# Kernel optimization log

Measured on AMD Instinct MI355X. Metric: run time of the kernel, lower is better.

Reference implementation:

```python
import jax, jax.numpy as jnp
import numpy as np

B, I, H, S = 16384, 256, 256, 32
EVENT_THRESH = 0.85


def setup_inputs() -> dict:
    key = jax.random.key(0)
    ks = jax.random.split(key, 20)
    r = lambda k, shp: jax.random.normal(k, shp, dtype=jnp.float32)
    w = lambda k, shp: jax.random.normal(k, shp, dtype=jnp.float32) * 0.02
    return {
        # forward args / state
        "x_t": r(ks[0], (B, I)),
        "h_lstm": r(ks[1], (B, H)),
        "c_lstm": r(ks[2], (B, H)),
        "h_mem_prev": jnp.zeros((B, H), jnp.float32),
        "slots": r(ks[3], (B, S, I)),
        "ptr": jax.random.randint(ks[4], (B,), 0, S, dtype=jnp.int64),
        # SequenceMemoryCell params (weights stored as (in, out))
        "W_val": w(ks[5], (I, I)),
        "b_val": jnp.zeros((I,), jnp.float32),
        "W_ev": w(ks[6], (I, 1)),
        "b_ev": jnp.zeros((1,), jnp.float32),
        "pos_emb": r(ks[7], (S, I)),
        "slot_weights": jnp.ones((S,), jnp.float32),
        "W_sp": w(ks[8], (I, H)),
        "b_sp": jnp.zeros((H,), jnp.float32),
        # LSTM params
        "W_ih": w(ks[9], (I + H, 4 * H)),
        "b_ih": jnp.zeros((4 * H,), jnp.float32),
        "W_hh": w(ks[10], (H, 4 * H)),
    }


def reference(x_t, h_lstm, c_lstm, h_mem_prev, slots, ptr,
              W_val, b_val, W_ev, b_ev, pos_emb, slot_weights, W_sp, b_sp,
              W_ih, b_ih, W_hh):
    n_slots = slot_weights.shape[0]
    # --- SequenceMemoryCell ---
    e_t = jax.nn.sigmoid(x_t @ W_ev + b_ev)            # (B, 1)
    v = x_t @ W_val + b_val                            # (B, I)
    event_mask = e_t[:, 0] > EVENT_THRESH              # (B,)
    # circular-buffer scatter write at ptr, gated by event_mask
    onehot = jnp.arange(n_slots)[None, :] == ptr[:, None]          # (B, S)
    write = event_mask[:, None] & onehot                           # (B, S)
    new_slots = jnp.where(write[:, :, None], v[:, None, :], slots) # (B, S, I)
    new_ptr = (ptr + event_mask.astype(ptr.dtype)) % n_slots
    # weighted pool over slots with positional embeddings
    w = jax.nn.softmax(slot_weights)                               # (S,)
    pooled = jnp.einsum('bsi,s->bi', new_slots + pos_emb[None], w) # (B, I)
    h_mem = pooled @ W_sp + b_sp                                   # (B, H)
    # --- LSTM on [x_t; h_mem] ---
    gates = jnp.concatenate([x_t, h_mem], axis=1) @ W_ih + b_ih + h_lstm @ W_hh
    i_g, f_g, g_t, o_g = jnp.split(gates, 4, axis=1)
    c_new = jax.nn.sigmoid(f_g) * c_lstm + jax.nn.sigmoid(i_g) * jnp.tanh(g_t)
    h_new = jax.nn.sigmoid(o_g) * jnp.tanh(c_new)
    return (h_new, c_new, h_mem, new_slots, new_ptr)
```

## Files before the change

kernel.cpp:

```cpp
#include <hip/hip_runtime.h>
#include <hip/hip_bf16.h>

#define B_SZ 16384
#define I_SZ 256
#define H_SZ 256
#define S_SZ 32

typedef __attribute__((ext_vector_type(8))) short short8;
typedef __attribute__((ext_vector_type(4))) float f32x4;

__device__ __forceinline__ ushort f2b(float f) {
  __hip_bfloat16 h = __float2bfloat16(f);
  return *reinterpret_cast<ushort*>(&h);
}
__device__ __forceinline__ float sgm(float x) { return 1.0f / (1.0f + expf(-x)); }

__device__ __forceinline__ void gll16(const void* g, void* l) {
  __builtin_amdgcn_global_load_lds(
      (const __attribute__((address_space(1))) unsigned*)g,
      (__attribute__((address_space(3))) unsigned*)l, 16, 0, 0);
}

__global__ __launch_bounds__(256) void prep_pe(
    const float* __restrict__ slot_w, const float* __restrict__ pos_emb,
    float* __restrict__ wsm_g, float* __restrict__ pe_g) {
  int t = threadIdx.x;
  __shared__ float w_sh[32];
  if (t < 32) {
    float v = slot_w[t];
    float m = v;
#pragma unroll
    for (int off = 16; off; off >>= 1) m = fmaxf(m, __shfl_xor(m, off));
    float e = expf(v - m);
    float s2 = e;
#pragma unroll
    for (int off = 16; off; off >>= 1) s2 += __shfl_xor(s2, off);
    float wv = e / s2;
    w_sh[t] = wv;
    wsm_g[t] = wv;
  }
  __syncthreads();
  float accp = 0.f;
#pragma unroll 8
  for (int s = 0; s < 32; s++) accp += w_sh[s] * pos_emb[s * 256 + t];
  pe_g[t] = accp;
}

__global__ __launch_bounds__(256, 6) void front(
    const float* __restrict__ x_t, const float* __restrict__ h_lstm,
    const float* __restrict__ slots, const int* __restrict__ ptr,
    const float* __restrict__ W_val, const float* __restrict__ b_val,
    const float* __restrict__ W_ev, const float* __restrict__ b_ev,
    const float* __restrict__ slot_w,
    const float* __restrict__ W_sp, const float* __restrict__ W_ih,
    const float* __restrict__ W_hh, const float* __restrict__ b_ih,
    const float* __restrict__ b_sp, const float* __restrict__ wsm_g,
    const float* __restrict__ pe_g,
    float* __restrict__ out_slots, float* __restrict__ out_ptr,
    ushort* __restrict__ x_b, ushort* __restrict__ hl_b,
    ushort* __restrict__ pooled_b, ushort* __restrict__ WspT,
    ushort* __restrict__ WcatT, float* __restrict__ biasp) {
  __shared__ float x_sh[4][256];
  __shared__ float w_sh[32];
  const int bid = blockIdx.x;
  const int t = threadIdx.x;

  if (bid < 4096) {
    int l = t & 63;
    int w = t >> 6;
    int b = bid * 4 + w;

    if (t < 32) w_sh[t] = wsm_g[t];
    f32x4 pev = *(const f32x4*)(pe_g + l * 4);

    float4 x4 = *(const float4*)(x_t + (size_t)b * 256 + l * 4);
    *(float4*)&x_sh[w][l * 4] = x4;
    ushort4 xb = make_ushort4(f2b(x4.x), f2b(x4.y), f2b(x4.z), f2b(x4.w));
    *(ushort4*)&x_b[(size_t)b * 256 + l * 4] = xb;
    float4 hl4 = *(const float4*)(h_lstm + (size_t)b * 256 + l * 4);
    ushort4 hb = make_ushort4(f2b(hl4.x), f2b(hl4.y), f2b(hl4.z), f2b(hl4.w));
    *(ushort4*)&hl_b[(size_t)b * 256 + l * 4] = hb;

    float4 we4 = *(const float4*)(W_ev + l * 4);
    float p = x4.x * we4.x + x4.y * we4.y + x4.z * we4.z + x4.w * we4.w;
    for (int off = 32; off; off >>= 1) p += __shfl_xor(p, off, 64);
    float z = p + b_ev[0];
    bool ev = sgm(z) > 0.85f;
    int pb = ptr[b];
    if (l == 0) out_ptr[b] = (float)(ev ? ((pb + 1) & 31) : pb);

    __syncthreads();

    f32x4 v4 = {0.f, 0.f, 0.f, 0.f};
    if (ev) {
      v4 = *(const f32x4*)(b_val + l * 4);
      for (int k = 0; k < 256; k++) {
        float xv = x_sh[w][k];
        f32x4 wv = *(const f32x4*)(W_val + (size_t)k * 256 + l * 4);
        v4 += xv * wv;
      }
    }

    const f32x4* sl4 = (const f32x4*)slots + (size_t)b * 2048;
    f32x4* os4 = (f32x4*)out_slots + (size_t)b * 2048;
    f32x4 pool = {0.f, 0.f, 0.f, 0.f};
#pragma unroll 8
    for (int s = 0; s < 32; s++) {
      f32x4 tv = __builtin_nontemporal_load(sl4 + s * 64 + l);
      if (ev && s == pb) tv = v4;
      __builtin_nontemporal_store(tv, os4 + s * 64 + l);
      pool += w_sh[s] * tv;
    }
    pool += pev;
    ushort4 pb4 = make_ushort4(f2b(pool[0]), f2b(pool[1]), f2b(pool[2]), f2b(pool[3]));
    *(ushort4*)&pooled_b[(size_t)b * 256 + l * 4] = pb4;

  } else if (bid < 4104) {
    for (int e = (bid - 4096) * 256 + t; e < 65536; e += 8 * 256) {
      int n = e >> 8, k = e & 255;
      WspT[e] = f2b(W_sp[k * 256 + n]);
    }
  } else if (bid < 4168) {
    for (int e = (bid - 4104) * 256 + t; e < 1024 * 512; e += 64 * 256) {
      int r = e >> 9, kk = e & 511;
      int k = (kk < 256) ? kk : kk + 256;
      int hb = r >> 6, g = (r >> 4) & 3, hl = r & 15;
      int n = g * 256 + hb * 16 + hl;
      float v = (k < 512) ? W_ih[(size_t)k * 1024 + n]
                          : W_hh[(size_t)(k - 512) * 1024 + n];
      WcatT[(size_t)r * 768 + k] = f2b(v);
    }
  } else if (bid < 4424) {
    int i = bid - 4168;
    x_sh[0][t] = W_sp[(size_t)i * 256 + t];
    __syncthreads();
    int n0 = t * 4;
    f32x4 acc = {0.f, 0.f, 0.f, 0.f};
    for (int m = 0; m < 256; m++) {
      float s = x_sh[0][m];
      f32x4 w2 = *(const f32x4*)(W_ih + (size_t)(256 + m) * 1024 + n0);
      acc += s * w2;
    }
#pragma unroll
    for (int d = 0; d < 4; d++) {
      int n = n0 + d;
      int g = n >> 8, rem = n & 255, hb = rem >> 4, hl = rem & 15;
      int r = hb * 64 + g * 16 + hl;
      WcatT[(size_t)r * 768 + 256 + i] = f2b(acc[d]);
    }
  } else {
    int n0 = t * 4;
    f32x4 acc = *(const f32x4*)(b_ih + n0);
    for (int m = 0; m < 256; m++) {
      float s = b_sp[m];
      f32x4 w2 = *(const f32x4*)(W_ih + (size_t)(256 + m) * 1024 + n0);
      acc += s * w2;
    }
    *(f32x4*)(biasp + n0) = acc;
  }
}

__global__ __launch_bounds__(256) void gemm_hmem(
    const ushort* __restrict__ A0, const ushort* __restrict__ WT,
    const float* __restrict__ bias, float* __restrict__ out_f32) {
  int l = threadIdx.x & 63;
  int wid = threadIdx.x >> 6;
  int wm = wid >> 1, wn = wid & 1;
  int m0 = blockIdx.x * 128;
  int n0 = blockIdx.y * 128;
  __shared__ ushort Ash[128 * 32];
  __shared__ ushort Bsh[128 * 32];

  f32x4 acc[4][4] = {};

  for (int k0 = 0; k0 < 256; k0 += 32) {
#pragma unroll
    for (int i = 0; i < 2; i++) {
      int seg = i * 256 + threadIdx.x;
      int row = seg >> 2, cb = (seg & 3) * 8;
      gll16(A0 + (size_t)(m0 + row) * 256 + k0 + cb, Ash + seg * 8);
    }
#pragma unroll
    for (int i = 0; i < 2; i++) {
      int seg = i * 256 + threadIdx.x;
      int row = seg >> 2, cb = (seg & 3) * 8;
      gll16(WT + (size_t)(n0 + row) * 256 + k0 + cb, Bsh + seg * 8);
    }
    __syncthreads();

    short8 af[4], bfr[4];
#pragma unroll
    for (int m = 0; m < 4; m++)
      af[m] = *(const short8*)&Ash[(wm * 64 + m * 16 + (l & 15)) * 32 + (l >> 4) * 8];
#pragma unroll
    for (int n = 0; n < 4; n++)
      bfr[n] = *(const short8*)&Bsh[(wn * 64 + n * 16 + (l & 15)) * 32 + (l >> 4) * 8];
#pragma unroll
    for (int m = 0; m < 4; m++)
#pragma unroll
      for (int n = 0; n < 4; n++)
        acc[m][n] = __builtin_amdgcn_mfma_f32_16x16x32_bf16(af[m], bfr[n], acc[m][n], 0, 0, 0);
    __syncthreads();
  }

#pragma unroll
  for (int m = 0; m < 4; m++)
#pragma unroll
    for (int n = 0; n < 4; n++)
#pragma unroll
      for (int r = 0; r < 4; r++) {
        int row = m0 + wm * 64 + m * 16 + (l >> 4) * 4 + r;
        int col = n0 + wn * 64 + n * 16 + (l & 15);
        out_f32[(size_t)row * 256 + col] = acc[m][n][r] + bias[col];
      }
}

template <int KTOT>
__global__ __launch_bounds__(512) void gemm256_lstm(
    const ushort* __restrict__ A0s, const ushort* __restrict__ A1s,
    const ushort* __restrict__ A2s, const ushort* __restrict__ WT,
    const float* __restrict__ bias, const float* __restrict__ c_lstm,
    float* __restrict__ h_out, float* __restrict__ c_out) {
  constexpr int NT = KTOT / 64;
  __shared__ ushort Ash[2][2][128][64];
  __shared__ ushort Bsh[2][2][128][64];
  const int tid = threadIdx.x;
  const int l = tid & 63;
  const int wid = tid >> 6;
  const int wm = wid >> 2, wn = wid & 3;
  const int id = blockIdx.x;
  const int xcd = id & 7, jj = id >> 3;
  const int mb = xcd * 8 + (jj >> 2), nb = jj & 3;
  const int m0 = mb * 256, n0 = nb * 256;

  auto asel = [&](int kt) { return kt < 4 ? A0s : (kt < 8 ? A1s : A2s); };

  auto stageA = [&](int bu, int h, int kt) {
    const ushort* s = asel(kt);
    int cb = (kt & 3) * 64;
#pragma unroll
    for (int ld = 0; ld < 2; ld++) {
      int seg = ld * 512 + tid;
      int row = seg >> 3, C = seg & 7;
      int Cs = C ^ (row & 7);
      gll16(s + (size_t)(m0 + h * 128 + row) * 256 + cb + Cs * 8,
            &Ash[bu][h][0][0] + seg * 8);
    }
  };
  auto stageB = [&](int bu, int h, int kt) {
    int cb = kt * 64;
#pragma unroll
    for (int ld = 0; ld < 2; ld++) {
      int seg = ld * 512 + tid;
      int row = seg >> 3, C = seg & 7;
      int Cs = C ^ (row & 7);
      gll16(WT + (size_t)(n0 + h * 128 + row) * KTOT + cb + Cs * 8,
            &Bsh[bu][h][0][0] + seg * 8);
    }
  };

  f32x4 acc[8][4] = {};

  stageB(0, 0, 0); stageB(0, 1, 0);
  stageA(0, 0, 0); stageA(0, 1, 0);
  stageB(1, 0, 1); stageB(1, 1, 1);

  for (int t = 0; t < NT; t++) {
    const int c = t & 1;
    const ushort* Abase = &Ash[c][wm][0][0];
    const ushort* Bbase = &Bsh[c][wn >> 1][0][0];

    if (t < NT - 1) asm volatile("s_waitcnt vmcnt(4)" ::: "memory");
    else            asm volatile("s_waitcnt vmcnt(0)" ::: "memory");
    asm volatile("s_barrier" ::: "memory");

    short8 bfr[4][2];
#pragma unroll
    for (int nf = 0; nf < 4; nf++)
#pragma unroll
      for (int kk = 0; kk < 2; kk++) {
        int r = (wn & 1) * 64 + nf * 16 + (l & 15);
        int C = (kk * 4 + (l >> 4)) ^ (l & 7);
        bfr[nf][kk] = *(const short8*)(Bbase + r * 64 + C * 8);
      }
    short8 af[2][2];
#pragma unroll
    for (int q = 0; q < 2; q++)
#pragma unroll
      for (int kk = 0; kk < 2; kk++) {
        int r = (0 * 2 + q) * 16 + (l & 15);
        int C = (kk * 4 + (l >> 4)) ^ (l & 7);
        af[q][kk] = *(const short8*)(Abase + r * 64 + C * 8);
      }
    if (t + 1 < NT) stageA(c ^ 1, 0, t + 1);
    __builtin_amdgcn_s_setprio(1);
#pragma unroll
    for (int q = 0; q < 2; q++)
#pragma unroll
      for (int nf = 0; nf < 4; nf++)
#pragma unroll
        for (int kk = 0; kk < 2; kk++)
          acc[q][nf] = __builtin_amdgcn_mfma_f32_16x16x32_bf16(
              af[q][kk], bfr[nf][kk], acc[q][nf], 0, 0, 0);
    __builtin_amdgcn_s_setprio(0);

#pragma unroll
    for (int p = 1; p < 4; p++) {
      asm volatile("s_barrier" ::: "memory");
#pragma unroll
      for (int q = 0; q < 2; q++)
#pragma unroll
        for (int kk = 0; kk < 2; kk++) {
          int r = (p * 2 + q) * 16 + (l & 15);
          int C = (kk * 4 + (l >> 4)) ^ (l & 7);
          af[q][kk] = *(const short8*)(Abase + r * 64 + C * 8);
        }
      if (p == 1) {
        if (t + 1 < NT) stageA(c ^ 1, 1, t + 1);
        if (t + 2 < NT) stageB(c, 0, t + 2);
      } else if (p == 2) {
        if (t + 2 < NT) stageB(c, 1, t + 2);
      }
      __builtin_amdgcn_s_setprio(1);
#pragma unroll
      for (int q = 0; q < 2; q++)
#pragma unroll
        for (int nf = 0; nf < 4; nf++)
#pragma unroll
          for (int kk = 0; kk < 2; kk++)
            acc[p * 2 + q][nf] = __builtin_amdgcn_mfma_f32_16x16x32_bf16(
                af[q][kk], bfr[nf][kk], acc[p * 2 + q][nf], 0, 0, 0);
      __builtin_amdgcn_s_setprio(0);
    }
  }

  int h = (nb * 4 + wn) * 16 + (l & 15);
  float bi = bias[h], bf_ = bias[256 + h], bg = bias[512 + h], bo = bias[768 + h];
#pragma unroll
  for (int mf = 0; mf < 8; mf++)
#pragma unroll
    for (int r = 0; r < 4; r++) {
      int row = m0 + wm * 128 + mf * 16 + (l >> 4) * 4 + r;
      float ig = acc[mf][0][r] + bi;
      float fg = acc[mf][1][r] + bf_;
      float gt = acc[mf][2][r] + bg;
      float og = acc[mf][3][r] + bo;
      float cc = c_lstm[(size_t)row * 256 + h];
      float cn = sgm(fg) * cc + sgm(ig) * tanhf(gt);
      float hn = sgm(og) * tanhf(cn);
      c_out[(size_t)row * 256 + h] = cn;
      h_out[(size_t)row * 256 + h] = hn;
    }
}

extern "C" void kernel_launch(void* const* d_in, const int* in_sizes, int n_in,
                              void* d_out, int out_size, void* d_ws, size_t ws_size,
                              hipStream_t stream) {
  const float* x_t    = (const float*)d_in[0];
  const float* h_lstm = (const float*)d_in[1];
  const float* c_lstm = (const float*)d_in[2];
  const float* slots  = (const float*)d_in[4];
  const int*   ptr    = (const int*)d_in[5];
  const float* W_val  = (const float*)d_in[6];
  const float* b_val  = (const float*)d_in[7];
  const float* W_ev   = (const float*)d_in[8];
  const float* b_ev   = (const float*)d_in[9];
  const float* pos_emb = (const float*)d_in[10];
  const float* slot_w  = (const float*)d_in[11];
  const float* W_sp   = (const float*)d_in[12];
  const float* b_sp   = (const float*)d_in[13];
  const float* W_ih   = (const float*)d_in[14];
  const float* b_ih   = (const float*)d_in[15];
  const float* W_hh   = (const float*)d_in[16];

  float* out = (float*)d_out;
  const size_t BH = (size_t)B_SZ * H_SZ;
  float* out_h    = out;
  float* out_c    = out + BH;
  float* out_hmem = out + 2 * BH;
  float* out_slots = out + 3 * BH;
  float* out_ptr   = out + 3 * BH + (size_t)B_SZ * S_SZ * I_SZ;

  char* ws = (char*)d_ws;
  ushort* x_b      = (ushort*)(ws);
  ushort* hl_b     = (ushort*)(ws + 8388608);
  ushort* pooled_b = (ushort*)(ws + 16777216);
  ushort* WspT     = (ushort*)(ws + 25165824);
  ushort* WcatT    = (ushort*)(ws + 25296896);
  float*  biasp    = (float*)(ws + 26869760);
  float*  wsm_g    = (float*)(ws + 26873856);
  float*  pe_g     = (float*)(ws + 26873984);

  prep_pe<<<1, 256, 0, stream>>>(slot_w, pos_emb, wsm_g, pe_g);

  front<<<4425, 256, 0, stream>>>(
      x_t, h_lstm, slots, ptr, W_val, b_val, W_ev, b_ev, slot_w,
      W_sp, W_ih, W_hh, b_ih, b_sp, wsm_g, pe_g,
      out_slots, out_ptr, x_b, hl_b, pooled_b, WspT, WcatT, biasp);

  gemm256_lstm<768><<<256, 512, 0, stream>>>(
      x_b, pooled_b, hl_b, WcatT, biasp, c_lstm, out_h, out_c);

  gemm_hmem<<<dim3(128, 2), 256, 0, stream>>>(
      pooled_b, WspT, b_sp, out_hmem);
}
```

Measured before the change: 254.0 us.

## Split front kernel into event/value kernel and separate slots copy-pool kernel

The monolithic front kernel is split in two. The first computes the event flag, the ptr update and the W_val projection (now using wave shuffles instead of LDS), and writes the event info and value vector to workspace. A new slots_copy kernel then streams the large slots tensor, applies the gated write and computes the pooled output, with softmax weights broadcast by shuffle. This is meant to keep the bandwidth-bound slots stream free of the compute-heavy value GEMV and its barrier, at the cost of an extra launch and a workspace round trip for the event flags and value vectors.

```diff
diff --git a/kernel.cpp b/kernel.cpp
--- a/kernel.cpp
+++ b/kernel.cpp
@@ -46,22 +46,20 @@
   pe_g[t] = accp;
 }
 
-__global__ __launch_bounds__(256, 6) void front(
+__global__ __launch_bounds__(256) void front_xh(
     const float* __restrict__ x_t, const float* __restrict__ h_lstm,
-    const float* __restrict__ slots, const int* __restrict__ ptr,
+    const int* __restrict__ ptr,
     const float* __restrict__ W_val, const float* __restrict__ b_val,
     const float* __restrict__ W_ev, const float* __restrict__ b_ev,
-    const float* __restrict__ slot_w,
     const float* __restrict__ W_sp, const float* __restrict__ W_ih,
     const float* __restrict__ W_hh, const float* __restrict__ b_ih,
-    const float* __restrict__ b_sp, const float* __restrict__ wsm_g,
-    const float* __restrict__ pe_g,
-    float* __restrict__ out_slots, float* __restrict__ out_ptr,
+    const float* __restrict__ b_sp,
+    float* __restrict__ out_ptr, float* __restrict__ evt,
+    float* __restrict__ vbuf,
     ushort* __restrict__ x_b, ushort* __restrict__ hl_b,
-    ushort* __restrict__ pooled_b, ushort* __restrict__ WspT,
-    ushort* __restrict__ WcatT, float* __restrict__ biasp) {
-  __shared__ float x_sh[4][256];
-  __shared__ float w_sh[32];
+    ushort* __restrict__ WspT, ushort* __restrict__ WcatT,
+    float* __restrict__ biasp) {
+  __shared__ float sh[256];
   const int bid = blockIdx.x;
   const int t = threadIdx.x;
 
@@ -70,11 +68,7 @@
     int w = t >> 6;
     int b = bid * 4 + w;
 
-    if (t < 32) w_sh[t] = wsm_g[t];
-    f32x4 pev = *(const f32x4*)(pe_g + l * 4);
-
     float4 x4 = *(const float4*)(x_t + (size_t)b * 256 + l * 4);
-    *(float4*)&x_sh[w][l * 4] = x4;
     ushort4 xb = make_ushort4(f2b(x4.x), f2b(x4.y), f2b(x4.z), f2b(x4.w));
     *(ushort4*)&x_b[(size_t)b * 256 + l * 4] = xb;
     float4 hl4 = *(const float4*)(h_lstm + (size_t)b * 256 + l * 4);
@@ -87,33 +81,23 @@
     float z = p + b_ev[0];
     bool ev = sgm(z) > 0.85f;
     int pb = ptr[b];
-    if (l == 0) out_ptr[b] = (float)(ev ? ((pb + 1) & 31) : pb);
-
-    __syncthreads();
-
-    f32x4 v4 = {0.f, 0.f, 0.f, 0.f};
+
     if (ev) {
-      v4 = *(const f32x4*)(b_val + l * 4);
-      for (int k = 0; k < 256; k++) {
-        float xv = x_sh[w][k];
-        f32x4 wv = *(const f32x4*)(W_val + (size_t)k * 256 + l * 4);
-        v4 += xv * wv;
+      f32x4 v4 = *(const f32x4*)(b_val + l * 4);
+      for (int k4 = 0; k4 < 64; k4++) {
+        float a0 = __shfl(x4.x, k4, 64), a1 = __shfl(x4.y, k4, 64);
+        float a2 = __shfl(x4.z, k4, 64), a3 = __shfl(x4.w, k4, 64);
+        v4 += a0 * (*(const f32x4*)(W_val + (size_t)(k4 * 4 + 0) * 256 + l * 4));
+        v4 += a1 * (*(const f32x4*)(W_val + (size_t)(k4 * 4 + 1) * 256 + l * 4));
+        v4 += a2 * (*(const f32x4*)(W_val + (size_t)(k4 * 4 + 2) * 256 + l * 4));
+        v4 += a3 * (*(const f32x4*)(W_val + (size_t)(k4 * 4 + 3) * 256 + l * 4));
       }
-    }
-
-    const f32x4* sl4 = (const f32x4*)slots + (size_t)b * 2048;
-    f32x4* os4 = (f32x4*)out_slots + (size_t)b * 2048;
-    f32x4 pool = {0.f, 0.f, 0.f, 0.f};
-#pragma unroll 8
-    for (int s = 0; s < 32; s++) {
-      f32x4 tv = __builtin_nontemporal_load(sl4 + s * 64 + l);
-      if (ev && s == pb) tv = v4;
-      __builtin_nontemporal_store(tv, os4 + s * 64 + l);
-      pool += w_sh[s] * tv;
-    }
-    pool += pev;
-    ushort4 pb4 = make_ushort4(f2b(pool[0]), f2b(pool[1]), f2b(pool[2]), f2b(pool[3]));
-    *(ushort4*)&pooled_b[(size_t)b * 256 + l * 4] = pb4;
+      *(f32x4*)(vbuf + (size_t)b * 256 + l * 4) = v4;
+    }
+    if (l == 0) {
+      out_ptr[b] = (float)(ev ? ((pb + 1) & 31) : pb);
+      evt[b] = ev ? (float)(pb + 1) : 0.0f;
+    }
 
   } else if (bid < 4104) {
     for (int e = (bid - 4096) * 256 + t; e < 65536; e += 8 * 256) {
@@ -132,12 +116,12 @@
     }
   } else if (bid < 4424) {
     int i = bid - 4168;
-    x_sh[0][t] = W_sp[(size_t)i * 256 + t];
+    sh[t] = W_sp[(size_t)i * 256 + t];
     __syncthreads();
     int n0 = t * 4;
     f32x4 acc = {0.f, 0.f, 0.f, 0.f};
     for (int m = 0; m < 256; m++) {
-      float s = x_sh[0][m];
+      float s = sh[m];
       f32x4 w2 = *(const f32x4*)(W_ih + (size_t)(256 + m) * 1024 + n0);
       acc += s * w2;
     }
@@ -158,6 +142,39 @@
     }
     *(f32x4*)(biasp + n0) = acc;
   }
+}
+
+__global__ __launch_bounds__(256) void slots_copy(
+    const float* __restrict__ slots, const float* __restrict__ evt,
+    const float* __restrict__ vbuf, const float* __restrict__ wsm_g,
+    const float* __restrict__ pe_g,
+    float* __restrict__ out_slots, ushort* __restrict__ pooled_b) {
+  int l = threadIdx.x & 63;
+  int w = threadIdx.x >> 6;
+  int b = blockIdx.x * 4 + w;
+
+  float wv = wsm_g[l & 31];
+  f32x4 pev = *(const f32x4*)(pe_g + l * 4);
+  float ef = evt[b];
+  bool ev = ef != 0.0f;
+  int pb = (int)ef - 1;
+
+  f32x4 v4 = {0.f, 0.f, 0.f, 0.f};
+  if (ev) v4 = *(const f32x4*)(vbuf + (size_t)b * 256 + l * 4);
+
+  const f32x4* sl4 = (const f32x4*)slots + (size_t)b * 2048 + l;
+  f32x4* os4 = (f32x4*)out_slots + (size_t)b * 2048 + l;
+  f32x4 pool = {0.f, 0.f, 0.f, 0.f};
+#pragma unroll 8
+  for (int s = 0; s < 32; s++) {
+    f32x4 tv = __builtin_nontemporal_load(sl4 + s * 64);
+    if (ev && s == pb) tv = v4;
+    __builtin_nontemporal_store(tv, os4 + s * 64);
+    pool += __shfl(wv, s, 64) * tv;
+  }
+  pool += pev;
+  ushort4 pb4 = make_ushort4(f2b(pool[0]), f2b(pool[1]), f2b(pool[2]), f2b(pool[3]));
+  *(ushort4*)&pooled_b[(size_t)b * 256 + l * 4] = pb4;
 }
 
 __global__ __launch_bounds__(256) void gemm_hmem(
@@ -390,13 +407,18 @@
   float*  biasp    = (float*)(ws + 26869760);
   float*  wsm_g    = (float*)(ws + 26873856);
   float*  pe_g     = (float*)(ws + 26873984);
+  float*  evt      = (float*)(ws + 26875904);
+  float*  vbuf     = (float*)(ws + 26941440);
 
   prep_pe<<<1, 256, 0, stream>>>(slot_w, pos_emb, wsm_g, pe_g);
 
-  front<<<4425, 256, 0, stream>>>(
-      x_t, h_lstm, slots, ptr, W_val, b_val, W_ev, b_ev, slot_w,
-      W_sp, W_ih, W_hh, b_ih, b_sp, wsm_g, pe_g,
-      out_slots, out_ptr, x_b, hl_b, pooled_b, WspT, WcatT, biasp);
+  front_xh<<<4425, 256, 0, stream>>>(
+      x_t, h_lstm, ptr, W_val, b_val, W_ev, b_ev,
+      W_sp, W_ih, W_hh, b_ih, b_sp,
+      out_ptr, evt, vbuf, x_b, hl_b, WspT, WcatT, biasp);
+
+  slots_copy<<<B_SZ / 4, 256, 0, stream>>>(
+      slots, evt, vbuf, wsm_g, pe_g, out_slots, pooled_b);
 
   gemm256_lstm<768><<<256, 512, 0, stream>>>(
       x_b, pooled_b, hl_b, WcatT, biasp, c_lstm, out_h, out_c);
```

Result: slower. 288.0 us (+13.4%).
